# Performance work log

Measured on AMD Instinct MI355X. Metric: run time of the kernel, lower is better.

Reference implementation:

```python
import jax, jax.numpy as jnp
import numpy as np

N_NODES = 50000
EMBED_DIM = 128
N_EDGES = 600000
ALPHA = 0.2  # LeakyReLU negative slope


def setup_inputs() -> dict:
    key = jax.random.key(0)
    k1, k2 = jax.random.split(key)
    drug_embeddings = jax.random.normal(k1, (N_NODES, EMBED_DIM), dtype=jnp.float32)
    drug_relationships = jax.random.randint(k2, (N_EDGES, 2), 0, N_NODES, dtype=jnp.int64)
    return {"drug_embeddings": drug_embeddings, "drug_relationships": drug_relationships}


def reference(drug_embeddings, drug_relationships):
    # edge_index = drug_relationships.T : row 0 = target/source node i, row 1 = neighbor j
    src = drug_relationships[:, 0]  # [E]
    dst = drug_relationships[:, 1]  # [E]
    drug_i = drug_embeddings[src]   # [E, D] gather
    drug_j = drug_embeddings[dst]   # [E, D] gather
    # per-edge dot-product score with LeakyReLU
    scores = jax.nn.leaky_relu(jnp.sum(drug_i * drug_j, axis=1), negative_slope=ALPHA)  # [E]
    # NOTE: original applies a single GLOBAL softmax over all edges (dim=0), not per-node
    att = jax.nn.softmax(scores, axis=0)  # [E]
    weighted = drug_j * att[:, None]      # [E, D]
    # scatter_add back onto source nodes
    h_prime = jax.ops.segment_sum(weighted, src, num_segments=drug_embeddings.shape[0])  # [N, D]
    return h_prime + drug_embeddings
```

## Files before the change

kernel.cpp:

```cpp
#include <hip/hip_runtime.h>
#include <math.h>

constexpr int kNodes = 50000;
constexpr int kEdges = 600000;
constexpr float kAlpha = 0.2f;
constexpr float kNegBig = -1e30f;

constexpr int kBlock = 256;
constexpr int kGrid  = 2048;
constexpr int kGStride = kGrid * kBlock;

constexpr int kGroups = 16;
constexpr int kBlocksPerGroup = kGrid / kGroups;

constexpr int kNodesPerBlock = 8;
constexpr int kNodeBlocks = kNodes / kNodesPerBlock;
constexpr int kMaxIt = (kNodeBlocks + kGrid - 1) / kGrid;

constexpr int kCap = 48;
constexpr int kWPN = kCap / 2;

constexpr int kOffRoot   = 16;
constexpr int kOffGrp    = 32;
constexpr int kOffCounts = kOffGrp + kGroups * 32;
constexpr int kOffCsr    = kOffCounts + kNodes;
constexpr int kOffPart   = kOffCsr + kNodes * kWPN;
constexpr int kEndWs     = kOffPart + 2 * kGrid;

__device__ __forceinline__ void gridBarrier(int* wsi, int ord) {
    __syncthreads();
    if (threadIdx.x == 0) {
        asm volatile("s_waitcnt vmcnt(0) lgkmcnt(0)" ::: "memory");
        const int grp = blockIdx.x & (kGroups - 1);
        int* gc = wsi + kOffGrp + grp * 32;
        const int old = __hip_atomic_fetch_add(gc, 1, __ATOMIC_RELAXED, __HIP_MEMORY_SCOPE_AGENT);
        if (old == kBlocksPerGroup * ord - 1)
            __hip_atomic_fetch_add(wsi + kOffRoot, 1, __ATOMIC_RELAXED, __HIP_MEMORY_SCOPE_AGENT);
        while (__hip_atomic_load(wsi + kOffRoot, __ATOMIC_RELAXED, __HIP_MEMORY_SCOPE_AGENT)
               < kGroups * ord)
            __builtin_amdgcn_s_sleep(4);
    }
    __syncthreads();
}

__device__ __forceinline__ void onlineMerge(float& m, float& s, float m2, float s2) {
    const float M = fmaxf(m, m2);
    s = s * __expf(m - M) + s2 * __expf(m2 - M);
    m = M;
}

__global__ __launch_bounds__(kBlock, 8)
void fused_kernel(const float4* __restrict__ emb4,
                  const int2*  __restrict__ rel2,
                  float4*      __restrict__ out4,
                  float*       __restrict__ wsf)
{
    int* wsi = (int*)wsf;
    int*                counts = wsi + kOffCounts;
    unsigned int*       csr32  = (unsigned int*)(wsi + kOffCsr);
    const unsigned int* csr32c = (const unsigned int*)(wsi + kOffCsr);

    const int tid  = threadIdx.x;
    const int gtid = blockIdx.x * kBlock + tid;

    for (int e = gtid; e < kEdges; e += kGStride) {
        const int2 sd = rel2[e];
        const int pos = atomicAdd(&counts[sd.x], 1);
        if (pos < kCap)
            atomicOr(&csr32[sd.x * kWPN + (pos >> 1)],
                     (unsigned int)sd.y << ((pos & 1) * 16));
    }
    gridBarrier(wsi, 1);

    const int g    = tid & 31;
    const int grp8 = tid >> 5;
    const char* embB = (const char*)emb4;
    const unsigned g16 = (unsigned)g * 16u;

    float4 accv[kMaxIt];
    float  mrun[kMaxIt];
    float Mgrp = kNegBig, Sgrp = 0.0f;

    #pragma unroll
    for (int it = 0; it < kMaxIt; ++it) {
        accv[it] = make_float4(0.f, 0.f, 0.f, 0.f);
        mrun[it] = kNegBig;
        const int vb = (int)blockIdx.x + it * kGrid;
        if (vb < kNodeBlocks) {
            const int node = vb * kNodesPerBlock + grp8;
            const float4 a = *(const float4*)(embB + ((unsigned)node * 512u + g16));
            float4 acc = make_float4(0.f, 0.f, 0.f, 0.f);
            float m_run = kNegBig, s_run = 0.0f;

            const int cnt = min(counts[node], kCap);
            unsigned int w = 0;
            if (g < kWPN && 2 * g < cnt)
                w = csr32c[node * kWPN + g];

            int k = 0;
            for (; k + 3 < cnt; k += 4) {
                const unsigned int w0 = __shfl(w, (k >> 1), 32);
                const unsigned int w1 = __shfl(w, (k >> 1) + 1, 32);
                const int d0 = (int)(w0 & 0xffffu), d1 = (int)(w0 >> 16);
                const int d2 = (int)(w1 & 0xffffu), d3 = (int)(w1 >> 16);
                const float4 b0 = *(const float4*)(embB + ((unsigned)d0 * 512u + g16));
                const float4 b1 = *(const float4*)(embB + ((unsigned)d1 * 512u + g16));
                const float4 b2 = *(const float4*)(embB + ((unsigned)d2 * 512u + g16));
                const float4 b3 = *(const float4*)(embB + ((unsigned)d3 * 512u + g16));
                float p0 = a.x*b0.x + a.y*b0.y + a.z*b0.z + a.w*b0.w;
                float p1 = a.x*b1.x + a.y*b1.y + a.z*b1.z + a.w*b1.w;
                float p2 = a.x*b2.x + a.y*b2.y + a.z*b2.z + a.w*b2.w;
                float p3 = a.x*b3.x + a.y*b3.y + a.z*b3.z + a.w*b3.w;
                #pragma unroll
                for (int o = 16; o > 0; o >>= 1) {
                    p0 += __shfl_xor(p0, o); p1 += __shfl_xor(p1, o);
                    p2 += __shfl_xor(p2, o); p3 += __shfl_xor(p3, o);
                }
                const float s0 = p0 > 0.f ? p0 : kAlpha * p0;
                const float s1 = p1 > 0.f ? p1 : kAlpha * p1;
                const float s2 = p2 > 0.f ? p2 : kAlpha * p2;
                const float s3 = p3 > 0.f ? p3 : kAlpha * p3;
                const float m4 = fmaxf(fmaxf(s0, s1), fmaxf(s2, s3));
                if (m4 > m_run) {
                    const float rs = __expf(m_run - m4);
                    s_run *= rs;
                    acc.x *= rs; acc.y *= rs; acc.z *= rs; acc.w *= rs;
                    m_run = m4;
                }
                const float w0e = __expf(s0 - m_run);
                const float w1e = __expf(s1 - m_run);
                const float w2e = __expf(s2 - m_run);
                const float w3e = __expf(s3 - m_run);
                s_run += w0e + w1e + w2e + w3e;
                acc.x += w0e*b0.x + w1e*b1.x + w2e*b2.x + w3e*b3.x;
                acc.y += w0e*b0.y + w1e*b1.y + w2e*b2.y + w3e*b3.y;
                acc.z += w0e*b0.z + w1e*b1.z + w2e*b2.z + w3e*b3.z;
                acc.w += w0e*b0.w + w1e*b1.w + w2e*b2.w + w3e*b3.w;
            }
            for (; k < cnt; ++k) {
                const unsigned int wk = __shfl(w, (k >> 1), 32);
                const int d0 = (int)((k & 1) ? (wk >> 16) : (wk & 0xffffu));
                const float4 b0 = *(const float4*)(embB + ((unsigned)d0 * 512u + g16));
                float p0 = a.x*b0.x + a.y*b0.y + a.z*b0.z + a.w*b0.w;
                #pragma unroll
                for (int o = 16; o > 0; o >>= 1) p0 += __shfl_xor(p0, o);
                const float s0 = p0 > 0.f ? p0 : kAlpha * p0;
                if (s0 > m_run) {
                    const float rs = __expf(m_run - s0);
                    s_run *= rs;
                    acc.x *= rs; acc.y *= rs; acc.z *= rs; acc.w *= rs;
                    m_run = s0;
                }
                const float w0e = __expf(s0 - m_run);
                s_run += w0e;
                acc.x += w0e*b0.x; acc.y += w0e*b0.y; acc.z += w0e*b0.z; acc.w += w0e*b0.w;
            }

            accv[it] = acc;
            mrun[it] = m_run;
            onlineMerge(Mgrp, Sgrp, m_run, s_run);
        }
    }

    __shared__ float sm[kNodesPerBlock];
    __shared__ float ss[kNodesPerBlock];
    if (g == 0) { sm[grp8] = Mgrp; ss[grp8] = Sgrp; }
    __syncthreads();
    if (tid == 0) {
        float M = sm[0], S = ss[0];
        #pragma unroll
        for (int i = 1; i < kNodesPerBlock; ++i) onlineMerge(M, S, sm[i], ss[i]);
        float2 p = make_float2(M, S);
        unsigned long long bits;
        __builtin_memcpy(&bits, &p, 8);
        __hip_atomic_store((unsigned long long*)(wsi + kOffPart) + blockIdx.x, bits,
                           __ATOMIC_RELAXED, __HIP_MEMORY_SCOPE_AGENT);
    }
    gridBarrier(wsi, 2);

    {
        float M = kNegBig, S = 0.0f;
        const float2* pp = (const float2*)(wsi + kOffPart);
        for (int i = tid; i < kGrid; i += kBlock) {
            const float2 p = pp[i];
            onlineMerge(M, S, p.x, p.y);
        }
        __shared__ float fm[kBlock];
        __shared__ float fs[kBlock];
        fm[tid] = M; fs[tid] = S;
        __syncthreads();
        for (int s = kBlock >> 1; s > 0; s >>= 1) {
            if (tid < s) {
                float m1 = fm[tid], s1 = fs[tid];
                onlineMerge(m1, s1, fm[tid + s], fs[tid + s]);
                fm[tid] = m1; fs[tid] = s1;
            }
            __syncthreads();
        }
        const float gM    = fm[0];
        const float gInvS = 1.0f / fs[0];

        char* outB = (char*)out4;
        #pragma unroll
        for (int it = 0; it < kMaxIt; ++it) {
            const int vb = (int)blockIdx.x + it * kGrid;
            if (vb < kNodeBlocks) {
                const int node = vb * kNodesPerBlock + grp8;
                const float scale = __expf(mrun[it] - gM) * gInvS;
                const float4 e4 = *(const float4*)(embB + ((unsigned)node * 512u + g16));
                const float4 o = accv[it];
                *(float4*)(outB + ((unsigned)node * 512u + g16)) =
                    make_float4(e4.x + scale * o.x, e4.y + scale * o.y,
                                e4.z + scale * o.z, e4.w + scale * o.w);
            }
        }
    }
}

extern "C" void kernel_launch(void* const* d_in, const int* in_sizes, int n_in,
                              void* d_out, int out_size, void* d_ws, size_t ws_size,
                              hipStream_t stream) {
    const float4* emb4 = (const float4*)d_in[0];
    const int2*   rel2 = (const int2*)d_in[1];
    float4* out4 = (float4*)d_out;
    float*  wsf  = (float*)d_ws;
    int*    wsi  = (int*)d_ws;

    hipMemsetAsync(wsi + kOffRoot, 0,
                   (size_t)(kOffPart - kOffRoot) * sizeof(int), stream);
    hipLaunchKernelGGL(fused_kernel, dim3(kGrid), dim3(kBlock), 0, stream,
                       emb4, rel2, out4, wsf);
}
```

Before: 193.7 us.

## Use full-int CSR without pre-zeroing, dynamic node-block scheduling, reuse self embedding

When the workspace is large enough, neighbor indices are stored as plain 32-bit ints with relaxed stores instead of packed 16-bit values written by atomicOr. That removes the atomics and the memset of the CSR region, so only the counters are cleared. Node blocks are now handed out through an atomic task counter, which balances work across blocks of unequal degree, at the cost of extra __syncthreads and one atomic per slot. Each thread also keeps its own embedding in registers, so the final output pass does not reload it, which adds register pressure.

```diff
diff --git a/kernel.cpp b/kernel.cpp
--- a/kernel.cpp
+++ b/kernel.cpp
@@ -15,17 +15,22 @@
 
 constexpr int kNodesPerBlock = 8;
 constexpr int kNodeBlocks = kNodes / kNodesPerBlock;
-constexpr int kMaxIt = (kNodeBlocks + kGrid - 1) / kGrid;
+constexpr int kSlots = 4;
 
 constexpr int kCap = 48;
 constexpr int kWPN = kCap / 2;
 
 constexpr int kOffRoot   = 16;
+constexpr int kOffTask   = 24;
 constexpr int kOffGrp    = 32;
 constexpr int kOffCounts = kOffGrp + kGroups * 32;
 constexpr int kOffCsr    = kOffCounts + kNodes;
-constexpr int kOffPart   = kOffCsr + kNodes * kWPN;
-constexpr int kEndWs     = kOffPart + 2 * kGrid;
+
+template <int IM> struct Lay {
+    static constexpr int csrWords = (IM == 0) ? kNodes * kWPN : kNodes * kCap;
+    static constexpr int offPart  = kOffCsr + csrWords;
+    static constexpr int endWs    = offPart + 2 * kGrid;
+};
 
 __device__ __forceinline__ void gridBarrier(int* wsi, int ord) {
     __syncthreads();
@@ -49,6 +54,7 @@
     m = M;
 }
 
+template <int IM>
 __global__ __launch_bounds__(kBlock, 8)
 void fused_kernel(const float4* __restrict__ emb4,
                   const int2*  __restrict__ rel2,
@@ -56,9 +62,9 @@
                   float*       __restrict__ wsf)
 {
     int* wsi = (int*)wsf;
-    int*                counts = wsi + kOffCounts;
-    unsigned int*       csr32  = (unsigned int*)(wsi + kOffCsr);
-    const unsigned int* csr32c = (const unsigned int*)(wsi + kOffCsr);
+    int*          counts = wsi + kOffCounts;
+    unsigned int* csrW   = (unsigned int*)(wsi + kOffCsr);
+    int*          csrI   = wsi + kOffCsr;
 
     const int tid  = threadIdx.x;
     const int gtid = blockIdx.x * kBlock + tid;
@@ -66,9 +72,14 @@
     for (int e = gtid; e < kEdges; e += kGStride) {
         const int2 sd = rel2[e];
         const int pos = atomicAdd(&counts[sd.x], 1);
-        if (pos < kCap)
-            atomicOr(&csr32[sd.x * kWPN + (pos >> 1)],
-                     (unsigned int)sd.y << ((pos & 1) * 16));
+        if (pos < kCap) {
+            if constexpr (IM == 0)
+                atomicOr(&csrW[sd.x * kWPN + (pos >> 1)],
+                         (unsigned int)sd.y << ((pos & 1) * 16));
+            else
+                __hip_atomic_store(&csrI[sd.x * kCap + pos], sd.y,
+                                   __ATOMIC_RELAXED, __HIP_MEMORY_SCOPE_AGENT);
+        }
     }
     gridBarrier(wsi, 1);
 
@@ -77,15 +88,24 @@
     const char* embB = (const char*)emb4;
     const unsigned g16 = (unsigned)g * 16u;
 
-    float4 accv[kMaxIt];
-    float  mrun[kMaxIt];
+    float4 accv[kSlots];
+    float4 aemb[kSlots];
+    float  mrun[kSlots];
+    int    vbs [kSlots];
     float Mgrp = kNegBig, Sgrp = 0.0f;
 
+    __shared__ int svb;
+
     #pragma unroll
-    for (int it = 0; it < kMaxIt; ++it) {
+    for (int it = 0; it < kSlots; ++it) {
+        if (tid == 0) svb = atomicAdd(wsi + kOffTask, 1);
+        __syncthreads();
+        const int vb = __builtin_amdgcn_readfirstlane(svb);
+        __syncthreads();
+        vbs[it]  = vb;
         accv[it] = make_float4(0.f, 0.f, 0.f, 0.f);
+        aemb[it] = make_float4(0.f, 0.f, 0.f, 0.f);
         mrun[it] = kNegBig;
-        const int vb = (int)blockIdx.x + it * kGrid;
         if (vb < kNodeBlocks) {
             const int node = vb * kNodesPerBlock + grp8;
             const float4 a = *(const float4*)(embB + ((unsigned)node * 512u + g16));
@@ -93,16 +113,24 @@
             float m_run = kNegBig, s_run = 0.0f;
 
             const int cnt = min(counts[node], kCap);
-            unsigned int w = 0;
-            if (g < kWPN && 2 * g < cnt)
-                w = csr32c[node * kWPN + g];
+            unsigned int lo = 0, hi = 0;
+            if (g < kWPN && 2 * g < cnt) {
+                if constexpr (IM == 0) {
+                    const unsigned int w = csrW[node * kWPN + g];
+                    lo = w & 0xffffu; hi = w >> 16;
+                } else {
+                    const int2 pr = *(const int2*)(csrI + node * kCap + 2 * g);
+                    lo = (unsigned int)pr.x; hi = (unsigned int)pr.y;
+                }
+            }
 
             int k = 0;
             for (; k + 3 < cnt; k += 4) {
-                const unsigned int w0 = __shfl(w, (k >> 1), 32);
-                const unsigned int w1 = __shfl(w, (k >> 1) + 1, 32);
-                const int d0 = (int)(w0 & 0xffffu), d1 = (int)(w0 >> 16);
-                const int d2 = (int)(w1 & 0xffffu), d3 = (int)(w1 >> 16);
+                const int h = k >> 1;
+                const int d0 = (int)__shfl(lo, h, 32);
+                const int d1 = (int)__shfl(hi, h, 32);
+                const int d2 = (int)__shfl(lo, h + 1, 32);
+                const int d3 = (int)__shfl(hi, h + 1, 32);
                 const float4 b0 = *(const float4*)(embB + ((unsigned)d0 * 512u + g16));
                 const float4 b1 = *(const float4*)(embB + ((unsigned)d1 * 512u + g16));
                 const float4 b2 = *(const float4*)(embB + ((unsigned)d2 * 512u + g16));
@@ -138,8 +166,8 @@
                 acc.w += w0e*b0.w + w1e*b1.w + w2e*b2.w + w3e*b3.w;
             }
             for (; k < cnt; ++k) {
-                const unsigned int wk = __shfl(w, (k >> 1), 32);
-                const int d0 = (int)((k & 1) ? (wk >> 16) : (wk & 0xffffu));
+                const unsigned int wv = (k & 1) ? hi : lo;
+                const int d0 = (int)__shfl(wv, k >> 1, 32);
                 const float4 b0 = *(const float4*)(embB + ((unsigned)d0 * 512u + g16));
                 float p0 = a.x*b0.x + a.y*b0.y + a.z*b0.z + a.w*b0.w;
                 #pragma unroll
@@ -157,6 +185,7 @@
             }
 
             accv[it] = acc;
+            aemb[it] = a;
             mrun[it] = m_run;
             onlineMerge(Mgrp, Sgrp, m_run, s_run);
         }
@@ -173,14 +202,14 @@
         float2 p = make_float2(M, S);
         unsigned long long bits;
         __builtin_memcpy(&bits, &p, 8);
-        __hip_atomic_store((unsigned long long*)(wsi + kOffPart) + blockIdx.x, bits,
+        __hip_atomic_store((unsigned long long*)(wsi + Lay<IM>::offPart) + blockIdx.x, bits,
                            __ATOMIC_RELAXED, __HIP_MEMORY_SCOPE_AGENT);
     }
     gridBarrier(wsi, 2);
 
     {
         float M = kNegBig, S = 0.0f;
-        const float2* pp = (const float2*)(wsi + kOffPart);
+        const float2* pp = (const float2*)(wsi + Lay<IM>::offPart);
         for (int i = tid; i < kGrid; i += kBlock) {
             const float2 p = pp[i];
             onlineMerge(M, S, p.x, p.y);
@@ -202,13 +231,12 @@
 
         char* outB = (char*)out4;
         #pragma unroll
-        for (int it = 0; it < kMaxIt; ++it) {
-            const int vb = (int)blockIdx.x + it * kGrid;
-            if (vb < kNodeBlocks) {
-                const int node = vb * kNodesPerBlock + grp8;
+        for (int it = 0; it < kSlots; ++it) {
+            if (vbs[it] < kNodeBlocks) {
+                const int node = vbs[it] * kNodesPerBlock + grp8;
                 const float scale = __expf(mrun[it] - gM) * gInvS;
-                const float4 e4 = *(const float4*)(embB + ((unsigned)node * 512u + g16));
-                const float4 o = accv[it];
+                const float4 e4 = aemb[it];
+                const float4 o  = accv[it];
                 *(float4*)(outB + ((unsigned)node * 512u + g16)) =
                     make_float4(e4.x + scale * o.x, e4.y + scale * o.y,
                                 e4.z + scale * o.z, e4.w + scale * o.w);
@@ -226,8 +254,15 @@
     float*  wsf  = (float*)d_ws;
     int*    wsi  = (int*)d_ws;
 
-    hipMemsetAsync(wsi + kOffRoot, 0,
-                   (size_t)(kOffPart - kOffRoot) * sizeof(int), stream);
-    hipLaunchKernelGGL(fused_kernel, dim3(kGrid), dim3(kBlock), 0, stream,
-                       emb4, rel2, out4, wsf);
-}
+    if (ws_size >= (size_t)Lay<1>::endWs * sizeof(int)) {
+        hipMemsetAsync(wsi + kOffRoot, 0,
+                       (size_t)(kOffCounts + kNodes - kOffRoot) * sizeof(int), stream);
+        hipLaunchKernelGGL((fused_kernel<1>), dim3(kGrid), dim3(kBlock), 0, stream,
+                           emb4, rel2, out4, wsf);
+    } else {
+        hipMemsetAsync(wsi + kOffRoot, 0,
+                       (size_t)(Lay<0>::offPart - kOffRoot) * sizeof(int), stream);
+        hipLaunchKernelGGL((fused_kernel<0>), dim3(kGrid), dim3(kBlock), 0, stream,
+                           emb4, rel2, out4, wsf);
+    }
+}
```

New measurement: 337.4 us. 1.74x slower.

## Centralize global softmax reduction in one block and cache node rows in LDS

Applied to the files above, without the earlier changes.

Only block 0 now reduces the per-block softmax partials. It publishes the global max and inverse sum through workspace, and a third grid barrier makes the other blocks wait before reading them. Each block no longer reads all 2048 partials, and the output epilogue reuses the self-embedding rows kept in shared memory instead of reloading them from global memory. The CSR neighbour words are also split into lo and hi halves before shuffling, to drop the mask and shift work per edge. The cost is an extra grid-wide barrier, more LDS use, and block 0 becoming a serial point.

```diff
diff --git a/kernel.cpp b/kernel.cpp
--- a/kernel.cpp
+++ b/kernel.cpp
@@ -20,6 +20,7 @@
 constexpr int kCap = 48;
 constexpr int kWPN = kCap / 2;
 
+constexpr int kOffFinal  = 8;
 constexpr int kOffRoot   = 16;
 constexpr int kOffGrp    = 32;
 constexpr int kOffCounts = kOffGrp + kGroups * 32;
@@ -81,6 +82,8 @@
     float  mrun[kMaxIt];
     float Mgrp = kNegBig, Sgrp = 0.0f;
 
+    __shared__ float4 aLds[kMaxIt][kNodesPerBlock][32];
+
     #pragma unroll
     for (int it = 0; it < kMaxIt; ++it) {
         accv[it] = make_float4(0.f, 0.f, 0.f, 0.f);
@@ -89,20 +92,24 @@
         if (vb < kNodeBlocks) {
             const int node = vb * kNodesPerBlock + grp8;
             const float4 a = *(const float4*)(embB + ((unsigned)node * 512u + g16));
+            aLds[it][grp8][g] = a;
             float4 acc = make_float4(0.f, 0.f, 0.f, 0.f);
             float m_run = kNegBig, s_run = 0.0f;
 
             const int cnt = min(counts[node], kCap);
-            unsigned int w = 0;
-            if (g < kWPN && 2 * g < cnt)
-                w = csr32c[node * kWPN + g];
+            unsigned int lo = 0, hi = 0;
+            if (g < kWPN && 2 * g < cnt) {
+                const unsigned int w = csr32c[node * kWPN + g];
+                lo = w & 0xffffu; hi = w >> 16;
+            }
 
             int k = 0;
             for (; k + 3 < cnt; k += 4) {
-                const unsigned int w0 = __shfl(w, (k >> 1), 32);
-                const unsigned int w1 = __shfl(w, (k >> 1) + 1, 32);
-                const int d0 = (int)(w0 & 0xffffu), d1 = (int)(w0 >> 16);
-                const int d2 = (int)(w1 & 0xffffu), d3 = (int)(w1 >> 16);
+                const int h = k >> 1;
+                const int d0 = (int)__shfl(lo, h, 32);
+                const int d1 = (int)__shfl(hi, h, 32);
+                const int d2 = (int)__shfl(lo, h + 1, 32);
+                const int d3 = (int)__shfl(hi, h + 1, 32);
                 const float4 b0 = *(const float4*)(embB + ((unsigned)d0 * 512u + g16));
                 const float4 b1 = *(const float4*)(embB + ((unsigned)d1 * 512u + g16));
                 const float4 b2 = *(const float4*)(embB + ((unsigned)d2 * 512u + g16));
@@ -138,8 +145,8 @@
                 acc.w += w0e*b0.w + w1e*b1.w + w2e*b2.w + w3e*b3.w;
             }
             for (; k < cnt; ++k) {
-                const unsigned int wk = __shfl(w, (k >> 1), 32);
-                const int d0 = (int)((k & 1) ? (wk >> 16) : (wk & 0xffffu));
+                const unsigned int wv = (k & 1) ? hi : lo;
+                const int d0 = (int)__shfl(wv, k >> 1, 32);
                 const float4 b0 = *(const float4*)(embB + ((unsigned)d0 * 512u + g16));
                 float p0 = a.x*b0.x + a.y*b0.y + a.z*b0.z + a.w*b0.w;
                 #pragma unroll
@@ -178,7 +185,7 @@
     }
     gridBarrier(wsi, 2);
 
-    {
+    if (blockIdx.x == 0) {
         float M = kNegBig, S = 0.0f;
         const float2* pp = (const float2*)(wsi + kOffPart);
         for (int i = tid; i < kGrid; i += kBlock) {
@@ -197,8 +204,28 @@
             }
             __syncthreads();
         }
-        const float gM    = fm[0];
-        const float gInvS = 1.0f / fs[0];
+        if (tid == 0) {
+            float2 fin = make_float2(fm[0], 1.0f / fs[0]);
+            unsigned long long bits;
+            __builtin_memcpy(&bits, &fin, 8);
+            __hip_atomic_store((unsigned long long*)(wsi + kOffFinal), bits,
+                               __ATOMIC_RELAXED, __HIP_MEMORY_SCOPE_AGENT);
+        }
+    }
+    gridBarrier(wsi, 3);
+
+    {
+        __shared__ float2 sfin;
+        if (tid == 0) {
+            const unsigned long long bits =
+                __hip_atomic_load((const unsigned long long*)(wsi + kOffFinal),
+                                  __ATOMIC_RELAXED, __HIP_MEMORY_SCOPE_AGENT);
+            float2 f; __builtin_memcpy(&f, &bits, 8);
+            sfin = f;
+        }
+        __syncthreads();
+        const float gM    = sfin.x;
+        const float gInvS = sfin.y;
 
         char* outB = (char*)out4;
         #pragma unroll
@@ -207,8 +234,8 @@
             if (vb < kNodeBlocks) {
                 const int node = vb * kNodesPerBlock + grp8;
                 const float scale = __expf(mrun[it] - gM) * gInvS;
-                const float4 e4 = *(const float4*)(embB + ((unsigned)node * 512u + g16));
-                const float4 o = accv[it];
+                const float4 e4 = aLds[it][grp8][g];
+                const float4 o  = accv[it];
                 *(float4*)(outB + ((unsigned)node * 512u + g16)) =
                     make_float4(e4.x + scale * o.x, e4.y + scale * o.y,
                                 e4.z + scale * o.z, e4.w + scale * o.w);
```

Measured after the change: 197.6 us. +2.0%, slower.
